# Kernel optimization log

Hardware: AMD Instinct MI355X
Metric: run time of the kernel (lower is better)

## Reference

```python
import jax, jax.numpy as jnp
import numpy as np

B, C, H, W = 4, 64, 128, 128
Q = 65536
OUT_SIZE = 256  # output image side -> cell = 2/OUT_SIZE
HIDDEN = 256
D_IN = C + 2 + 2  # feat + rel_coord + rel_cell


def setup_inputs() -> dict:
    key = jax.random.key(0)
    ks = jax.random.split(key, 8)
    feat = jax.random.normal(ks[0], (B, C, H, W), dtype=jnp.float32)
    coord = jax.random.uniform(ks[1], (B, Q, 2), dtype=jnp.float32, minval=-1.0, maxval=1.0)
    cell = jnp.full((B, Q, 2), 2.0 / OUT_SIZE, dtype=jnp.float32)

    def lin(k, din, dout):
        return jax.random.normal(k, (din, dout), dtype=jnp.float32) * (1.0 / np.sqrt(din))

    w0 = lin(ks[2], D_IN, HIDDEN)
    w1 = lin(ks[3], HIDDEN, HIDDEN)
    w2 = lin(ks[4], HIDDEN, HIDDEN)
    w3 = lin(ks[5], HIDDEN, HIDDEN)
    w4 = lin(ks[6], HIDDEN, 3)
    z = lambda d: jnp.zeros((d,), dtype=jnp.float32)
    return {"feat": feat, "coord": coord, "cell": cell,
            "w0": w0, "b0": z(HIDDEN), "w1": w1, "b1": z(HIDDEN),
            "w2": w2, "b2": z(HIDDEN), "w3": w3, "b3": z(HIDDEN),
            "w4": w4, "b4": z(3)}


def _liif(feat, coord, cell, ws, bs):
    b, c, h, w = feat.shape
    eps = 1e-6
    rx, ry = 1.0 / h, 1.0 / w  # 2/h/2, 2/w/2
    # local ensemble shifts, loop order vx outer, vy inner: (-1,-1),(-1,1),(1,-1),(1,1)
    shifts = jnp.array([[-rx, -ry], [-rx, ry], [rx, -ry], [rx, ry]], dtype=feat.dtype) + eps
    feat_flat = feat.reshape(b, c, h * w)
    cell_scale = jnp.array([h, w], dtype=feat.dtype)
    rel_cell = cell * cell_scale  # same for all branches

    def branch(shift):
        cshift = jnp.clip(coord + shift, -1.0 + eps, 1.0 - eps)
        # nearest grid_sample, align_corners=False: idx = floor((x+1)*size/2), clamped
        iy = jnp.clip(jnp.floor((cshift[..., 0] + 1.0) * (h * 0.5)), 0.0, h - 1.0).astype(jnp.int32)
        ix = jnp.clip(jnp.floor((cshift[..., 1] + 1.0) * (w * 0.5)), 0.0, w - 1.0).astype(jnp.int32)
        idx = iy * w + ix  # [B, Q]
        q_feat = jnp.take_along_axis(feat_flat, idx[:, None, :], axis=2)  # [B, C, Q]
        q_feat = q_feat.transpose(0, 2, 1)  # [B, Q, C]
        # feat_coord at the gathered pixel (make_coord values)
        qc0 = -1.0 + (2.0 * iy.astype(feat.dtype) + 1.0) / h
        qc1 = -1.0 + (2.0 * ix.astype(feat.dtype) + 1.0) / w
        rel0 = (coord[..., 0] - qc0) * h
        rel1 = (coord[..., 1] - qc1) * w
        inp = jnp.concatenate([q_feat, rel0[..., None], rel1[..., None], rel_cell], axis=-1)
        x = inp
        for wi, bi in zip(ws[:-1], bs[:-1]):
            x = jax.nn.relu(x @ wi + bi)
        pred = x @ ws[-1] + bs[-1]  # [B, Q, 3]
        area = jnp.abs(rel0 * rel1) + 1e-9  # [B, Q]
        return pred, area

    preds, areas = jax.vmap(branch)(shifts)  # [4,B,Q,3], [4,B,Q]
    tot = areas.sum(axis=0)
    # diagonal weight swap: 0<->3, 1<->2  == reverse
    wgt = areas[::-1] / tot
    return (preds * wgt[..., None]).sum(axis=0)  # [B, Q, 3]


def reference(feat, coord, cell, w0, b0, w1, b1, w2, b2, w3, b3, w4, b4):
    ws = [w0, w1, w2, w3, w4]
    bs = [b0, b1, b2, b3, b4]
    return _liif(feat, coord, cell, ws, bs)
```

## Files before the change

### kernel.cpp

```cpp
#include <hip/hip_runtime.h>
#include <cstdint>

typedef __bf16 bf16x8 __attribute__((ext_vector_type(8)));
typedef float f32x4 __attribute__((ext_vector_type(4)));
typedef unsigned int u32x4 __attribute__((ext_vector_type(4)));
typedef unsigned int u32x2 __attribute__((ext_vector_type(2)));
typedef unsigned short u16;
typedef unsigned int u32;

#define HH 128
#define WW 128
#define CC 64
#define QQ 65536
#define BB 4

#define RS 264

#define L0_OFF 0
#define L1_OFF 24576
#define L2_OFF 90112
#define L3_OFF 155648
#define W4_OFF 221184
#define FEATT_BYTE_OFF 524288u

__global__ void pack_weights(const float* __restrict__ w0,
                             const float* __restrict__ w1,
                             const float* __restrict__ w2,
                             const float* __restrict__ w3,
                             const float* __restrict__ w4,
                             u16* __restrict__ ws_us) {
    int bid = blockIdx.x;
    int lane = threadIdx.x;
    int tile, nk, off, Ksrc, Ncols, NT;
    const float* w;
    if (bid < 48)       { tile = bid;       nk = 3; off = L0_OFF; w = w0; Ksrc = 68;  Ncols = 256; NT = 16; }
    else if (bid < 176) { tile = bid - 48;  nk = 8; off = L1_OFF; w = w1; Ksrc = 256; Ncols = 256; NT = 16; }
    else if (bid < 304) { tile = bid - 176; nk = 8; off = L2_OFF; w = w2; Ksrc = 256; Ncols = 256; NT = 16; }
    else if (bid < 432) { tile = bid - 304; nk = 8; off = L3_OFF; w = w3; Ksrc = 256; Ncols = 256; NT = 16; }
    else                { tile = bid - 432; nk = 8; off = W4_OFF; w = w4; Ksrc = 256; Ncols = 3;   NT = 1;  }
    int kt = tile % nk;
    int nt = tile / nk;
    int n = nt * 16 + (lane & 15);
    int kbase = kt * 32 + (lane >> 4) * 8;
    unsigned int d[4];
    for (int i = 0; i < 4; ++i) {
        unsigned int lo, hi;
        {
            int k = kbase + 2 * i;
            float x = (k < Ksrc && n < Ncols) ? w[k * Ncols + n] : 0.0f;
            __bf16 hb = (__bf16)x;
            lo = (unsigned int)__builtin_bit_cast(u16, hb);
        }
        {
            int k = kbase + 2 * i + 1;
            float x = (k < Ksrc && n < Ncols) ? w[k * Ncols + n] : 0.0f;
            __bf16 hb = (__bf16)x;
            hi = (unsigned int)__builtin_bit_cast(u16, hb);
        }
        d[i] = lo | (hi << 16);
    }
    u32x4 pk = { d[0], d[1], d[2], d[3] };
    int dst = off + (kt * NT + nt) * 512 + lane * 8;
    *reinterpret_cast<u32x4*>(ws_us + dst) = pk;
}

__global__ void prep_featT(const float* __restrict__ feat, u16* __restrict__ featT) {
    __shared__ u16 tile[128 * 66];
    int bid = blockIdx.x;
    int b = bid >> 7, y = bid & 127;
    for (int idx = threadIdx.x; idx < CC * WW; idx += 256) {
        int c = idx >> 7, x = idx & 127;
        float v = feat[(((b * CC + c) * HH + y) * WW) + x];
        __bf16 hb = (__bf16)v;
        tile[x * 66 + c] = __builtin_bit_cast(u16, hb);
    }
    __syncthreads();
    for (int idx = threadIdx.x; idx < 2048; idx += 256) {
        int x = idx >> 4, c4 = (idx & 15) * 4;
        const u16* src = tile + x * 66 + c4;
        u32x2 d;
        d[0] = (unsigned int)src[0] | ((unsigned int)src[1] << 16);
        d[1] = (unsigned int)src[2] | ((unsigned int)src[3] << 16);
        *reinterpret_cast<u32x2*>(featT + ((b * HH + y) * WW + x) * CC + c4) = d;
    }
}

__device__ __forceinline__ void preload_w(u32x4 wpre[4], const u32x4* __restrict__ wbase,
                                          int voff) {
#pragma unroll
    for (int fi = 0; fi < 4; ++fi)
        wpre[fi] = wbase[voff + fi * 64];
}

template <int NK>
__device__ __forceinline__ void gemm_layer(u16* buf,
                                           const u32x4* __restrict__ wbase,
                                           const float* __restrict__ bias,
                                           int wave, int lane,
                                           const u32x4 wpre[4],
                                           u32x4 wnxt[4],
                                           const u32x4* __restrict__ wnb,
                                           int vnxt) {
    f32x4 acc[4][4] = {};
    const int l15 = lane & 15;
    const int qd = lane >> 4;
    const int voff = wave * 256 + lane;
    const u16* xb = buf + l15 * RS + qd * 8;
    u16* db = buf + l15 * RS + wave * 64 + qd * 4;

    u32x4 wq[2][4];
#pragma unroll
    for (int fi = 0; fi < 4; ++fi) wq[0][fi] = wpre[fi];

    bf16x8 xc[4];
#pragma unroll
    for (int st = 0; st < 4; ++st)
        xc[st] = __builtin_bit_cast(bf16x8,
            *reinterpret_cast<const u32x4*>(xb + st * 16 * RS));

#pragma unroll
    for (int kt = 0; kt < NK; ++kt) {
        if (kt + 1 < NK) {
            const u32x4* wn = wbase + (kt + 1) * 1024;
#pragma unroll
            for (int fi = 0; fi < 4; ++fi)
                wq[(kt + 1) & 1][fi] = wn[voff + fi * 64];
        }
#pragma unroll
        for (int st = 0; st < 4; ++st) {
#pragma unroll
            for (int fi = 0; fi < 4; ++fi)
                acc[fi][st] = __builtin_amdgcn_mfma_f32_16x16x32_bf16(
                    __builtin_bit_cast(bf16x8, wq[kt & 1][fi]), xc[st],
                    acc[fi][st], 0, 0, 0);
            if (kt + 1 < NK)
                xc[st] = __builtin_bit_cast(bf16x8,
                    *reinterpret_cast<const u32x4*>(xb + st * 16 * RS + (kt + 1) * 32));
        }
    }

#pragma unroll
    for (int fi = 0; fi < 4; ++fi) wnxt[fi] = wnb[vnxt + fi * 64];

    __syncthreads();

#pragma unroll
    for (int fi = 0; fi < 4; ++fi) {
        int fbase = (wave * 4 + fi) * 16 + qd * 4;
        f32x4 bv = *reinterpret_cast<const f32x4*>(bias + fbase);
#pragma unroll
        for (int st = 0; st < 4; ++st) {
            float v0 = fmaxf(acc[fi][st][0] + bv[0], 0.0f);
            float v1 = fmaxf(acc[fi][st][1] + bv[1], 0.0f);
            float v2 = fmaxf(acc[fi][st][2] + bv[2], 0.0f);
            float v3 = fmaxf(acc[fi][st][3] + bv[3], 0.0f);
            __bf16 h0 = (__bf16)v0, h1 = (__bf16)v1, h2 = (__bf16)v2, h3 = (__bf16)v3;
            u32x2 d;
            d[0] = (u32)__builtin_bit_cast(u16, h0) | ((u32)__builtin_bit_cast(u16, h1) << 16);
            d[1] = (u32)__builtin_bit_cast(u16, h2) | ((u32)__builtin_bit_cast(u16, h3) << 16);
            *reinterpret_cast<u32x2*>(db + st * 16 * RS + fi * 16) = d;
        }
    }
}

__global__ __launch_bounds__(256, 4) void liif_main(
    const float* __restrict__ coord, const float* __restrict__ cell,
    const float* __restrict__ b0, const float* __restrict__ b1,
    const float* __restrict__ b2, const float* __restrict__ b3,
    const float* __restrict__ b4,
    const u16* __restrict__ wpack, const u16* __restrict__ featT,
    float* __restrict__ out) {
    __shared__ u16 bufA[64 * RS];
    __shared__ float areasLDS[64];

    const int t = threadIdx.x;
    const int wave = t >> 6, lane = t & 63;
    const int row = t >> 2, p = t & 3;

    const int bq = blockIdx.x * 16 + (row >> 2);
    const int v = row & 3;
    const int b = bq >> 16;
    const float c0 = coord[bq * 2 + 0];
    const float c1 = coord[bq * 2 + 1];
    const float rc0 = cell[bq * 2 + 0] * 128.0f;
    const float rc1 = cell[bq * 2 + 1] * 128.0f;
    const float eps = 1e-6f;
    const float sx = ((v & 2) ? 0.0078125f : -0.0078125f) + eps;
    const float sy = ((v & 1) ? 0.0078125f : -0.0078125f) + eps;
    float cs0 = fminf(fmaxf(c0 + sx, -1.0f + eps), 1.0f - eps);
    float cs1 = fminf(fmaxf(c1 + sy, -1.0f + eps), 1.0f - eps);
    float fy = fminf(fmaxf(floorf((cs0 + 1.0f) * 64.0f), 0.0f), 127.0f);
    float fx = fminf(fmaxf(floorf((cs1 + 1.0f) * 64.0f), 0.0f), 127.0f);
    int iy = (int)fy, ix = (int)fx;
    float qc0 = -1.0f + (2.0f * fy + 1.0f) * 0.0078125f;
    float qc1 = -1.0f + (2.0f * fx + 1.0f) * 0.0078125f;
    float rel0 = (c0 - qc0) * 128.0f;
    float rel1 = (c1 - qc1) * 128.0f;
    float area = fabsf(rel0 * rel1) + 1e-9f;

    {
        const u16* fr = featT + (((b * HH + iy) * WW + ix) * CC) + p * 16;
        u32x4 f0 = *reinterpret_cast<const u32x4*>(fr);
        u32x4 f1 = *reinterpret_cast<const u32x4*>(fr + 8);
        u16* sb = bufA + row * RS;
        *reinterpret_cast<u32x4*>(sb + p * 16) = f0;
        *reinterpret_cast<u32x4*>(sb + p * 16 + 8) = f1;
        u32x4 e = { 0u, 0u, 0u, 0u };
        if (p == 0) {
            __bf16 h0 = (__bf16)rel0, h1 = (__bf16)rel1, h2 = (__bf16)rc0, h3 = (__bf16)rc1;
            e[0] = (u32)__builtin_bit_cast(u16, h0) | ((u32)__builtin_bit_cast(u16, h1) << 16);
            e[1] = (u32)__builtin_bit_cast(u16, h2) | ((u32)__builtin_bit_cast(u16, h3) << 16);
            areasLDS[row] = area;
        }
        *reinterpret_cast<u32x4*>(sb + 64 + p * 8) = e;
    }

    const u32x4* wp = reinterpret_cast<const u32x4*>(wpack);
    const u32x4* wp0 = wp + (L0_OFF / 8);
    const u32x4* wp1 = wp + (L1_OFF / 8);
    const u32x4* wp2 = wp + (L2_OFF / 8);
    const u32x4* wp3 = wp + (L3_OFF / 8);
    const u32x4* wp4 = wp + (W4_OFF / 8);
    const int voff = wave * 256 + lane;

    u32x4 wA[4], wB[4];
    preload_w(wA, wp0, voff);
    __syncthreads();
    gemm_layer<3>(bufA, wp0, b0, wave, lane, wA, wB, wp1, voff);
    __syncthreads();
    gemm_layer<8>(bufA, wp1, b1, wave, lane, wB, wA, wp2, voff);
    __syncthreads();
    gemm_layer<8>(bufA, wp2, b2, wave, lane, wA, wB, wp3, voff);
    __syncthreads();
    gemm_layer<8>(bufA, wp3, b3, wave, lane, wB, wA, wp4, lane);
    u32x4 w4hi[4];
#pragma unroll
    for (int kt = 0; kt < 4; ++kt) w4hi[kt] = wp4[(kt + 4) * 64 + lane];
    __syncthreads();

    const int l15 = lane & 15;
    const int qd = lane >> 4;
    const u16* xb = bufA + (wave * 16 + l15) * RS + qd * 8;
    f32x4 accf = {};
#pragma unroll
    for (int kt = 0; kt < 4; ++kt) {
        bf16x8 x = __builtin_bit_cast(bf16x8,
            *reinterpret_cast<const u32x4*>(xb + kt * 32));
        accf = __builtin_amdgcn_mfma_f32_16x16x32_bf16(
            __builtin_bit_cast(bf16x8, wA[kt]), x, accf, 0, 0, 0);
    }
#pragma unroll
    for (int kt = 4; kt < 8; ++kt) {
        bf16x8 x = __builtin_bit_cast(bf16x8,
            *reinterpret_cast<const u32x4*>(xb + kt * 32));
        accf = __builtin_amdgcn_mfma_f32_16x16x32_bf16(
            __builtin_bit_cast(bf16x8, w4hi[kt - 4]), x, accf, 0, 0, 0);
    }
    float a = areasLDS[wave * 16 + l15];
    float a1 = a + __shfl_xor(a, 1);
    float asum = a1 + __shfl_xor(a1, 2);
    float aopp = __shfl_xor(a, 3);
    float wgt = aopp / asum;
    float o0 = (accf[0] + b4[0]) * wgt;
    float o1 = (accf[1] + b4[1]) * wgt;
    float o2 = (accf[2] + b4[2]) * wgt;
    o0 += __shfl_xor(o0, 1); o0 += __shfl_xor(o0, 2);
    o1 += __shfl_xor(o1, 1); o1 += __shfl_xor(o1, 2);
    o2 += __shfl_xor(o2, 1); o2 += __shfl_xor(o2, 2);

    if (qd == 0 && (l15 & 3) == 0) {
        int obq = blockIdx.x * 16 + wave * 4 + (l15 >> 2);
        out[obq * 3 + 0] = o0;
        out[obq * 3 + 1] = o1;
        out[obq * 3 + 2] = o2;
    }
}

extern "C" void kernel_launch(void* const* d_in, const int* in_sizes, int n_in,
                              void* d_out, int out_size, void* d_ws, size_t ws_size,
                              hipStream_t stream) {
    const float* feat  = (const float*)d_in[0];
    const float* coord = (const float*)d_in[1];
    const float* cell  = (const float*)d_in[2];
    const float* w0 = (const float*)d_in[3];
    const float* b0 = (const float*)d_in[4];
    const float* w1 = (const float*)d_in[5];
    const float* b1 = (const float*)d_in[6];
    const float* w2 = (const float*)d_in[7];
    const float* b2 = (const float*)d_in[8];
    const float* w3 = (const float*)d_in[9];
    const float* b3 = (const float*)d_in[10];
    const float* w4 = (const float*)d_in[11];
    const float* b4 = (const float*)d_in[12];

    u16* ws_us = (u16*)d_ws;
    u16* featT = (u16*)((char*)d_ws + FEATT_BYTE_OFF);

    hipLaunchKernelGGL(pack_weights, dim3(440), dim3(64), 0, stream,
                       w0, w1, w2, w3, w4, ws_us);
    hipLaunchKernelGGL(prep_featT, dim3(BB * HH), dim3(256), 0, stream, feat, featT);
    hipLaunchKernelGGL(liif_main, dim3((BB * QQ) / 16), dim3(256), 0, stream,
                       coord, cell, b0, b1, b2, b3, b4, ws_us, featT,
                       (float*)d_out);
}
```

Measured before the change: 531.1 us.

## Switch MLP hidden layers to 32x32x16 bf16 MFMA with repacked weights

```diff
diff --git a/kernel.cpp b/kernel.cpp
--- a/kernel.cpp
+++ b/kernel.cpp
@@ -3,6 +3,7 @@
 
 typedef __bf16 bf16x8 __attribute__((ext_vector_type(8)));
 typedef float f32x4 __attribute__((ext_vector_type(4)));
+typedef float f32x16 __attribute__((ext_vector_type(16)));
 typedef unsigned int u32x4 __attribute__((ext_vector_type(4)));
 typedef unsigned int u32x2 __attribute__((ext_vector_type(2)));
 typedef unsigned short u16;
@@ -17,10 +18,10 @@
 #define RS 264
 
 #define L0_OFF 0
-#define L1_OFF 24576
-#define L2_OFF 90112
-#define L3_OFF 155648
-#define W4_OFF 221184
+#define L1_OFF 20480
+#define L2_OFF 86016
+#define L3_OFF 151552
+#define W4_OFF 217088
 #define FEATT_BYTE_OFF 524288u
 
 __global__ void pack_weights(const float* __restrict__ w0,
@@ -31,17 +32,26 @@
                              u16* __restrict__ ws_us) {
     int bid = blockIdx.x;
     int lane = threadIdx.x;
-    int tile, nk, off, Ksrc, Ncols, NT;
+    int dst, kbase, n, Ksrc, Ncols;
     const float* w;
-    if (bid < 48)       { tile = bid;       nk = 3; off = L0_OFF; w = w0; Ksrc = 68;  Ncols = 256; NT = 16; }
-    else if (bid < 176) { tile = bid - 48;  nk = 8; off = L1_OFF; w = w1; Ksrc = 256; Ncols = 256; NT = 16; }
-    else if (bid < 304) { tile = bid - 176; nk = 8; off = L2_OFF; w = w2; Ksrc = 256; Ncols = 256; NT = 16; }
-    else if (bid < 432) { tile = bid - 304; nk = 8; off = L3_OFF; w = w3; Ksrc = 256; Ncols = 256; NT = 16; }
-    else                { tile = bid - 432; nk = 8; off = W4_OFF; w = w4; Ksrc = 256; Ncols = 3;   NT = 1;  }
-    int kt = tile % nk;
-    int nt = tile / nk;
-    int n = nt * 16 + (lane & 15);
-    int kbase = kt * 32 + (lane >> 4) * 8;
+    if (bid < 424) {
+        int tile, off;
+        if (bid < 40)       { tile = bid;       off = L0_OFF; w = w0; Ksrc = 68;  }
+        else if (bid < 168) { tile = bid - 40;  off = L1_OFF; w = w1; Ksrc = 256; }
+        else if (bid < 296) { tile = bid - 168; off = L2_OFF; w = w2; Ksrc = 256; }
+        else                { tile = bid - 296; off = L3_OFF; w = w3; Ksrc = 256; }
+        int nt = tile & 7, ks = tile >> 3;
+        n = nt * 32 + (lane & 31);
+        kbase = ks * 16 + (lane >> 5) * 8;
+        Ncols = 256;
+        dst = off + tile * 512 + lane * 8;
+    } else {
+        int kt = bid - 424;
+        n = lane & 15;
+        kbase = kt * 32 + (lane >> 4) * 8;
+        w = w4; Ksrc = 256; Ncols = 3;
+        dst = W4_OFF + kt * 512 + lane * 8;
+    }
     unsigned int d[4];
     for (int i = 0; i < 4; ++i) {
         unsigned int lo, hi;
@@ -60,7 +70,6 @@
         d[i] = lo | (hi << 16);
     }
     u32x4 pk = { d[0], d[1], d[2], d[3] };
-    int dst = off + (kt * NT + nt) * 512 + lane * 8;
     *reinterpret_cast<u32x4*>(ws_us + dst) = pk;
 }
 
@@ -85,80 +94,86 @@
     }
 }
 
-__device__ __forceinline__ void preload_w(u32x4 wpre[4], const u32x4* __restrict__ wbase,
-                                          int voff) {
-#pragma unroll
-    for (int fi = 0; fi < 4; ++fi)
-        wpre[fi] = wbase[voff + fi * 64];
-}
-
-template <int NK>
-__device__ __forceinline__ void gemm_layer(u16* buf,
-                                           const u32x4* __restrict__ wbase,
-                                           const float* __restrict__ bias,
-                                           int wave, int lane,
-                                           const u32x4 wpre[4],
-                                           u32x4 wnxt[4],
-                                           const u32x4* __restrict__ wnb,
-                                           int vnxt) {
-    f32x4 acc[4][4] = {};
-    const int l15 = lane & 15;
-    const int qd = lane >> 4;
-    const int voff = wave * 256 + lane;
-    const u16* xb = buf + l15 * RS + qd * 8;
-    u16* db = buf + l15 * RS + wave * 64 + qd * 4;
-
-    u32x4 wq[2][4];
-#pragma unroll
-    for (int fi = 0; fi < 4; ++fi) wq[0][fi] = wpre[fi];
-
-    bf16x8 xc[4];
-#pragma unroll
-    for (int st = 0; st < 4; ++st)
-        xc[st] = __builtin_bit_cast(bf16x8,
-            *reinterpret_cast<const u32x4*>(xb + st * 16 * RS));
-
-#pragma unroll
-    for (int kt = 0; kt < NK; ++kt) {
-        if (kt + 1 < NK) {
-            const u32x4* wn = wbase + (kt + 1) * 1024;
-#pragma unroll
-            for (int fi = 0; fi < 4; ++fi)
-                wq[(kt + 1) & 1][fi] = wn[voff + fi * 64];
-        }
-#pragma unroll
-        for (int st = 0; st < 4; ++st) {
-#pragma unroll
-            for (int fi = 0; fi < 4; ++fi)
-                acc[fi][st] = __builtin_amdgcn_mfma_f32_16x16x32_bf16(
-                    __builtin_bit_cast(bf16x8, wq[kt & 1][fi]), xc[st],
-                    acc[fi][st], 0, 0, 0);
-            if (kt + 1 < NK)
-                xc[st] = __builtin_bit_cast(bf16x8,
-                    *reinterpret_cast<const u32x4*>(xb + st * 16 * RS + (kt + 1) * 32));
-        }
-    }
-
-#pragma unroll
-    for (int fi = 0; fi < 4; ++fi) wnxt[fi] = wnb[vnxt + fi * 64];
-
-    __syncthreads();
-
-#pragma unroll
-    for (int fi = 0; fi < 4; ++fi) {
-        int fbase = (wave * 4 + fi) * 16 + qd * 4;
-        f32x4 bv = *reinterpret_cast<const f32x4*>(bias + fbase);
-#pragma unroll
-        for (int st = 0; st < 4; ++st) {
-            float v0 = fmaxf(acc[fi][st][0] + bv[0], 0.0f);
-            float v1 = fmaxf(acc[fi][st][1] + bv[1], 0.0f);
-            float v2 = fmaxf(acc[fi][st][2] + bv[2], 0.0f);
-            float v3 = fmaxf(acc[fi][st][3] + bv[3], 0.0f);
-            __bf16 h0 = (__bf16)v0, h1 = (__bf16)v1, h2 = (__bf16)v2, h3 = (__bf16)v3;
-            u32x2 d;
-            d[0] = (u32)__builtin_bit_cast(u16, h0) | ((u32)__builtin_bit_cast(u16, h1) << 16);
-            d[1] = (u32)__builtin_bit_cast(u16, h2) | ((u32)__builtin_bit_cast(u16, h3) << 16);
-            *reinterpret_cast<u32x2*>(db + st * 16 * RS + fi * 16) = d;
+__device__ __forceinline__ void preload32(u32x4 w[4], const u32x4* __restrict__ b,
+                                          int v) {
+    w[0] = b[v];
+    w[1] = b[v + 64];
+    w[2] = b[v + 512];
+    w[3] = b[v + 576];
+}
+
+template <int NKS>
+__device__ __forceinline__ void gemm32(u16* buf,
+                                       const u32x4* __restrict__ wbase,
+                                       const float* __restrict__ bias,
+                                       int wave, int lane,
+                                       const u32x4 wpre[4],
+                                       u32x4 wnxt[4],
+                                       const u32x4* __restrict__ wnb,
+                                       int vnxt, int nstride2) {
+    f32x16 acc[2][2] = {};
+    const int l31 = lane & 31;
+    const int hi = lane >> 5;
+    const int voff = wave * 128 + lane;
+    const u16* xb = buf + l31 * RS + hi * 8;
+    u16* db = buf + l31 * RS + wave * 64 + hi * 4;
+
+    u32x4 wq[2][2];
+    wq[0][0] = wpre[0]; wq[0][1] = wpre[1];
+    wq[1][0] = wpre[2]; wq[1][1] = wpre[3];
+
+    bf16x8 xc[2];
+    xc[0] = __builtin_bit_cast(bf16x8, *reinterpret_cast<const u32x4*>(xb));
+    xc[1] = __builtin_bit_cast(bf16x8, *reinterpret_cast<const u32x4*>(xb + 32 * RS));
+
+#pragma unroll
+    for (int ks = 0; ks < NKS; ++ks) {
+        acc[0][0] = __builtin_amdgcn_mfma_f32_32x32x16_bf16(
+            __builtin_bit_cast(bf16x8, wq[ks & 1][0]), xc[0], acc[0][0], 0, 0, 0);
+        acc[1][0] = __builtin_amdgcn_mfma_f32_32x32x16_bf16(
+            __builtin_bit_cast(bf16x8, wq[ks & 1][1]), xc[0], acc[1][0], 0, 0, 0);
+        if (ks + 1 < NKS)
+            xc[0] = __builtin_bit_cast(bf16x8,
+                *reinterpret_cast<const u32x4*>(xb + (ks + 1) * 16));
+        acc[0][1] = __builtin_amdgcn_mfma_f32_32x32x16_bf16(
+            __builtin_bit_cast(bf16x8, wq[ks & 1][0]), xc[1], acc[0][1], 0, 0, 0);
+        acc[1][1] = __builtin_amdgcn_mfma_f32_32x32x16_bf16(
+            __builtin_bit_cast(bf16x8, wq[ks & 1][1]), xc[1], acc[1][1], 0, 0, 0);
+        if (ks + 1 < NKS)
+            xc[1] = __builtin_bit_cast(bf16x8,
+                *reinterpret_cast<const u32x4*>(xb + 32 * RS + (ks + 1) * 16));
+        if (ks + 2 < NKS) {
+            const u32x4* wn = wbase + (ks + 2) * 512;
+            wq[ks & 1][0] = wn[voff];
+            wq[ks & 1][1] = wn[voff + 64];
+        }
+    }
+
+    wnxt[0] = wnb[vnxt];
+    wnxt[1] = wnb[vnxt + 64];
+    wnxt[2] = wnb[vnxt + nstride2];
+    wnxt[3] = wnb[vnxt + nstride2 + 64];
+
+    __syncthreads();
+
+#pragma unroll
+    for (int ft = 0; ft < 2; ++ft) {
+        const int fb = wave * 64 + ft * 32 + hi * 4;
+#pragma unroll
+        for (int q4 = 0; q4 < 4; ++q4) {
+            f32x4 bv = *reinterpret_cast<const f32x4*>(bias + fb + q4 * 8);
+#pragma unroll
+            for (int st = 0; st < 2; ++st) {
+                float v0 = fmaxf(acc[ft][st][q4 * 4 + 0] + bv[0], 0.0f);
+                float v1 = fmaxf(acc[ft][st][q4 * 4 + 1] + bv[1], 0.0f);
+                float v2 = fmaxf(acc[ft][st][q4 * 4 + 2] + bv[2], 0.0f);
+                float v3 = fmaxf(acc[ft][st][q4 * 4 + 3] + bv[3], 0.0f);
+                __bf16 h0 = (__bf16)v0, h1 = (__bf16)v1, h2 = (__bf16)v2, h3 = (__bf16)v3;
+                u32x2 d;
+                d[0] = (u32)__builtin_bit_cast(u16, h0) | ((u32)__builtin_bit_cast(u16, h1) << 16);
+                d[1] = (u32)__builtin_bit_cast(u16, h2) | ((u32)__builtin_bit_cast(u16, h3) << 16);
+                *reinterpret_cast<u32x2*>(db + st * 32 * RS + ft * 32 + q4 * 8) = d;
+            }
         }
     }
 }
@@ -221,18 +236,18 @@
     const u32x4* wp2 = wp + (L2_OFF / 8);
     const u32x4* wp3 = wp + (L3_OFF / 8);
     const u32x4* wp4 = wp + (W4_OFF / 8);
-    const int voff = wave * 256 + lane;
+    const int voff = wave * 128 + lane;
 
     u32x4 wA[4], wB[4];
-    preload_w(wA, wp0, voff);
-    __syncthreads();
-    gemm_layer<3>(bufA, wp0, b0, wave, lane, wA, wB, wp1, voff);
-    __syncthreads();
-    gemm_layer<8>(bufA, wp1, b1, wave, lane, wB, wA, wp2, voff);
-    __syncthreads();
-    gemm_layer<8>(bufA, wp2, b2, wave, lane, wA, wB, wp3, voff);
-    __syncthreads();
-    gemm_layer<8>(bufA, wp3, b3, wave, lane, wB, wA, wp4, lane);
+    preload32(wA, wp0, voff);
+    __syncthreads();
+    gemm32<5>(bufA, wp0, b0, wave, lane, wA, wB, wp1, voff, 512);
+    __syncthreads();
+    gemm32<16>(bufA, wp1, b1, wave, lane, wB, wA, wp2, voff, 512);
+    __syncthreads();
+    gemm32<16>(bufA, wp2, b2, wave, lane, wA, wB, wp3, voff, 512);
+    __syncthreads();
+    gemm32<16>(bufA, wp3, b3, wave, lane, wB, wA, wp4, lane, 128);
     u32x4 w4hi[4];
 #pragma unroll
     for (int kt = 0; kt < 4; ++kt) w4hi[kt] = wp4[(kt + 4) * 64 + lane];
@@ -296,7 +311,7 @@
     u16* ws_us = (u16*)d_ws;
     u16* featT = (u16*)((char*)d_ws + FEATT_BYTE_OFF);
 
-    hipLaunchKernelGGL(pack_weights, dim3(440), dim3(64), 0, stream,
+    hipLaunchKernelGGL(pack_weights, dim3(432), dim3(64), 0, stream,
                        w0, w1, w2, w3, w4, ws_us);
     hipLaunchKernelGGL(prep_featT, dim3(BB * HH), dim3(256), 0, stream, feat, featT);
     hipLaunchKernelGGL(liif_main, dim3((BB * QQ) / 16), dim3(256), 0, stream,
```

After: 550.3 us. 1.04x slower.
